# Performance work log

Measured on AMD Instinct MI355X. Metric: run time of the kernel, lower is better.

Reference implementation:

```python
import jax, jax.numpy as jnp
import numpy as np

EPS = 1e-8
BOX2D_IDX = jnp.array([0, 1, 3, 4, 6])  # x, y, dx, dy, yaw


def box2corners(box):
    # box: (..., 5) = (x, y, w, h, alpha) -> corners (..., 4, 2), CCW order
    x, y, w, h, a = (box[..., i] for i in range(5))
    tx = jnp.array([0.5, -0.5, -0.5, 0.5], box.dtype)
    ty = jnp.array([0.5, 0.5, -0.5, -0.5], box.dtype)
    x4 = tx * w[..., None]
    y4 = ty * h[..., None]
    c, s = jnp.cos(a)[..., None], jnp.sin(a)[..., None]
    rx = c * x4 - s * y4 + x[..., None]
    ry = s * x4 + c * y4 + y[..., None]
    return jnp.stack([rx, ry], axis=-1)


def edge_intersections(c1, c2):
    # all 4x4 edge-edge intersections of two quads -> pts (..., 16, 2), mask (..., 16)
    p1 = c1[..., :, None, :]
    p2 = jnp.roll(c1, -1, axis=-2)[..., :, None, :]
    q1 = c2[..., None, :, :]
    q2 = jnp.roll(c2, -1, axis=-2)[..., None, :, :]
    r = p2 - p1
    s = q2 - q1
    denom = r[..., 0] * s[..., 1] - r[..., 1] * s[..., 0]
    safe = jnp.where(jnp.abs(denom) < EPS, 1.0, denom)
    qp = q1 - p1
    t = (qp[..., 0] * s[..., 1] - qp[..., 1] * s[..., 0]) / safe
    u = (qp[..., 0] * r[..., 1] - qp[..., 1] * r[..., 0]) / safe
    mask = (jnp.abs(denom) > EPS) & (t > 0) & (t < 1) & (u > 0) & (u < 1)
    pts = jnp.where(mask[..., None], p1 + t[..., None] * r, 0.0)
    lead = pts.shape[:-3]
    return pts.reshape(lead + (16, 2)), mask.reshape(lead + (16,))


def points_in_box(pts, corners):
    # pts (..., K, 2) inside rotated quad given by corners (..., 4, 2) -> (..., K) bool
    a = corners[..., 0:1, :]
    ab = corners[..., 1:2, :] - a
    ad = corners[..., 3:4, :] - a
    ap = pts - a
    pab = jnp.sum(ap * ab, -1)
    pad = jnp.sum(ap * ad, -1)
    nab = jnp.sum(ab * ab, -1)
    nad = jnp.sum(ad * ad, -1)
    return (pab > 0) & (pab < nab) & (pad > 0) & (pad < nad)


def masked_polygon_area(verts, mask):
    # verts (..., 24, 2) candidate vertices, mask (..., 24) validity
    m = mask.astype(verts.dtype)
    num = jnp.maximum(jnp.sum(m, -1, keepdims=True), 1.0)
    mean = jnp.sum(verts * m[..., None], -2, keepdims=True) / num[..., None]
    d = verts - mean  # centered (shoelace is translation-invariant)
    ang = jnp.arctan2(d[..., 1], d[..., 0])
    # push invalid vertices to the end with stable tie-break
    ang = jnp.where(mask, ang, 1e6 + jnp.arange(24, dtype=ang.dtype))
    idx = jnp.argsort(ang, axis=-1)
    vs = jnp.take_along_axis(d, idx[..., None], axis=-2)
    ms = jnp.take_along_axis(mask, idx, axis=-1)
    v0 = vs[..., 0:1, :]
    vs = jnp.where(ms[..., None], vs, v0)  # collapse invalid onto first vertex
    nxt = jnp.roll(vs, -1, axis=-2)
    cross = vs[..., 0] * nxt[..., 1] - vs[..., 1] * nxt[..., 0]
    return 0.5 * jnp.abs(jnp.sum(cross, -1))


def rotated_iou_3d(b1, b2):
    # b1, b2: (..., 7) = (x, y, z, dx, dy, dz, yaw); elementwise-aligned IoU
    c1 = box2corners(b1[..., BOX2D_IDX])
    c2 = box2corners(b2[..., BOX2D_IDX])
    ipts, imask = edge_intersections(c1, c2)
    in1 = points_in_box(c1, c2)
    in2 = points_in_box(c2, c1)
    verts = jnp.concatenate([c1, c2, ipts], axis=-2)  # (..., 24, 2)
    mask = jnp.concatenate([in1, in2, imask], axis=-1)
    inter2d = masked_polygon_area(verts, mask)
    zmax = jnp.minimum(b1[..., 2] + 0.5 * b1[..., 5], b2[..., 2] + 0.5 * b2[..., 5])
    zmin = jnp.maximum(b1[..., 2] - 0.5 * b1[..., 5], b2[..., 2] - 0.5 * b2[..., 5])
    inter3d = inter2d * jnp.maximum(zmax - zmin, 0.0)
    v1 = b1[..., 3] * b1[..., 4] * b1[..., 5]
    v2 = b2[..., 3] * b2[..., 4] * b2[..., 5]
    return inter3d / (v1 + v2 - inter3d + EPS)


def setup_inputs() -> dict:
    key = jax.random.key(0)
    k1, k2, k3, k4, k5 = jax.random.split(key, 5)
    N = 1048576
    ctr = (jax.random.uniform(k1, (N, 3)) - 0.5) * 40.0
    dims = jax.random.uniform(k2, (N, 3)) * 2.0 + 0.5
    yaw = (jax.random.uniform(k3, (N, 1)) - 0.5) * (2.0 * np.pi)
    pred = jnp.concatenate([ctr, dims, yaw], axis=-1).astype(jnp.float32)
    noise = jax.random.normal(k4, (N, 7)) * jnp.array(
        [0.3, 0.3, 0.3, 0.2, 0.2, 0.2, 0.2], jnp.float32)
    target = pred + noise
    target = target.at[:, 3:6].set(jnp.maximum(target[:, 3:6], 0.1))
    weight = jax.random.uniform(k5, (N,), dtype=jnp.float32)
    return {"pred": pred, "target": target, "weight": weight}


def reference(pred, target, weight):
    # IoU3DLoss(with_yaw=True, reduction='mean', loss_weight=1.0)
    loss_weight = 1.0
    iou = rotated_iou_3d(pred[None, ...], target[None, ...])  # (1, N)
    iou_loss = (1.0 - iou) * weight
    return loss_weight * jnp.mean(iou_loss)
```

## Files before the change

kernel.cpp:

```cpp
#include <hip/hip_runtime.h>

#define EPS_F 1e-8f
#define EPT 4

typedef float vf4 __attribute__((ext_vector_type(4)));

__device__ __forceinline__ vf4 load4u(const float* p) {
    vf4 v;
    __builtin_memcpy(&v, p, 16);
    return v;
}

__device__ __forceinline__ float fast_rcp(float x) {
    return __builtin_amdgcn_rcpf(x);
}

__global__ void zero_out_kernel(float* out) { out[0] = 0.f; }

__device__ __forceinline__ float edge_contrib(float ax, float ay,
                                              float bx, float by,
                                              float W, float H) {
    float dx = bx - ax, dy = by - ay;
    float sdx = (fabsf(dx) < 1e-20f) ? 1e-20f : dx;
    float sdy = (fabsf(dy) < 1e-20f) ? 1e-20f : dy;
    float rdx = fast_rcp(sdx);
    float rdy = fast_rcp(sdy);

    float tA = (-W - ax) * rdx;
    float tB = ( W - ax) * rdx;
    float ta = fmaxf(fminf(tA, tB), 0.f);
    float tb = fminf(fmaxf(tA, tB), 1.f);
    tb = fmaxf(ta, tb);

    float u0 = (-H - ay) * rdy;
    float u1 = ( H - ay) * rdy;
    float tm0 = fminf(u0, u1), tm1 = fmaxf(u0, u1);
    float t1 = fminf(fmaxf(tm0, ta), tb);
    float t2 = fminf(fmaxf(tm1, ta), tb);

    float x0 = fmaf(ta, dx, ax), y0 = fmaf(ta, dy, ay);
    float x1 = fmaf(t1, dx, ax), y1 = fmaf(t1, dy, ay);
    float x2 = fmaf(t2, dx, ax), y2 = fmaf(t2, dy, ay);
    float x3 = fmaf(tb, dx, ax), y3 = fmaf(tb, dy, ay);
    float h0 = fminf(fmaxf(y0, -H), H) + H;
    float h1 = fminf(fmaxf(y1, -H), H) + H;
    float h2 = fminf(fmaxf(y2, -H), H) + H;
    float h3 = fminf(fmaxf(y3, -H), H) + H;

    return (x1 - x0) * (h0 + h1) + (x2 - x1) * (h1 + h2) + (x3 - x2) * (h2 + h3);
}

__global__ __launch_bounds__(256, 4) void iou3d_loss_kernel(
    const float* __restrict__ pred, const float* __restrict__ target,
    const float* __restrict__ weight, float* __restrict__ out,
    int N, float invN)
{
    int base = blockIdx.x * (256 * EPT) + threadIdx.x;

    vf4 A0[EPT], A1[EPT], B0[EPT], B1[EPT];
    float wgt[EPT];
    #pragma unroll
    for (int e = 0; e < EPT; ++e) {
        int i = base + e * 256;
        int j = (i < N) ? i : 0;
        long o = (long)j * 7;
        A0[e] = load4u(pred + o);
        A1[e] = load4u(pred + o + 3);
        B0[e] = load4u(target + o);
        B1[e] = load4u(target + o + 3);
        wgt[e] = (i < N) ? weight[j] : 0.f;
    }

    float val = 0.f;
    #pragma unroll
    for (int e = 0; e < EPT; ++e) {
        float s1, c1, s2, c2;
        __sincosf(A1[e].w, &s1, &c1);
        __sincosf(B1[e].w, &s2, &c2);
        float cd = c1 * c2 + s1 * s2;
        float sd = c1 * s2 - s1 * c2;
        float dxc = B0[e].x - A0[e].x, dyc = B0[e].y - A0[e].y;
        float tx =  c1 * dxc + s1 * dyc;
        float ty = -s1 * dxc + c1 * dyc;
        float W = 0.5f * A1[e].x, H = 0.5f * A1[e].y;
        float w2 = 0.5f * B1[e].x, h2 = 0.5f * B1[e].y;

        float cw = cd * w2, sw = sd * w2, ch = cd * h2, sh = sd * h2;
        float q0x =  cw - sh + tx, q0y =  sw + ch + ty;
        float q1x = -cw - sh + tx, q1y = -sw + ch + ty;
        float q2x = -cw + sh + tx, q2y = -sw - ch + ty;
        float q3x =  cw + sh + tx, q3y =  sw - ch + ty;

        float s  = edge_contrib(q0x, q0y, q1x, q1y, W, H)
                 + edge_contrib(q1x, q1y, q2x, q2y, W, H)
                 + edge_contrib(q2x, q2y, q3x, q3y, W, H)
                 + edge_contrib(q3x, q3y, q0x, q0y, W, H);
        float area = 0.5f * fabsf(s);

        float zmax = fminf(A0[e].z + 0.5f * A1[e].z, B0[e].z + 0.5f * B1[e].z);
        float zmin = fmaxf(A0[e].z - 0.5f * A1[e].z, B0[e].z - 0.5f * B1[e].z);
        float inter3d = area * fmaxf(zmax - zmin, 0.f);
        float v1 = A1[e].x * A1[e].y * A1[e].z;
        float v2 = B1[e].x * B1[e].y * B1[e].z;
        float iou = inter3d * fast_rcp(v1 + v2 - inter3d + EPS_F);
        val += (1.f - iou) * wgt[e];
    }

    #pragma unroll
    for (int off = 32; off > 0; off >>= 1) val += __shfl_down(val, off, 64);
    __shared__ float wsum[4];
    int lane = threadIdx.x & 63, wid = threadIdx.x >> 6;
    if (lane == 0) wsum[wid] = val;
    __syncthreads();
    if (threadIdx.x == 0) {
        float ssum = (wsum[0] + wsum[1] + wsum[2] + wsum[3]) * invN;
        atomicAdd(out, ssum);
    }
}

extern "C" void kernel_launch(void* const* d_in, const int* in_sizes, int n_in,
                              void* d_out, int out_size, void* d_ws, size_t ws_size,
                              hipStream_t stream) {
    const float* pred   = (const float*)d_in[0];
    const float* target = (const float*)d_in[1];
    const float* weight = (const float*)d_in[2];
    float* out = (float*)d_out;
    int N = in_sizes[2];

    zero_out_kernel<<<1, 1, 0, stream>>>(out);
    int block = 256;
    int grid = (N + block * EPT - 1) / (block * EPT);
    iou3d_loss_kernel<<<grid, block, 0, stream>>>(pred, target, weight, out,
                                                  N, 1.f / (float)N);
}
```

Baseline: 102.8 us.

## Stage pred/target slabs through LDS with coalesced 16-byte loads

```diff
diff --git a/kernel.cpp b/kernel.cpp
--- a/kernel.cpp
+++ b/kernel.cpp
@@ -1,15 +1,13 @@
 #include <hip/hip_runtime.h>
 
 #define EPS_F 1e-8f
-#define EPT 4
+#define BLOCK 256
+#define EPT 2
+#define ELEMS (BLOCK * EPT)
+#define SLAB_DW (ELEMS * 7)
+#define SLAB_CH (SLAB_DW / 4)
 
 typedef float vf4 __attribute__((ext_vector_type(4)));
-
-__device__ __forceinline__ vf4 load4u(const float* p) {
-    vf4 v;
-    __builtin_memcpy(&v, p, 16);
-    return v;
-}
 
 __device__ __forceinline__ float fast_rcp(float x) {
     return __builtin_amdgcn_rcpf(x);
@@ -50,40 +48,61 @@
     return (x1 - x0) * (h0 + h1) + (x2 - x1) * (h1 + h2) + (x3 - x2) * (h2 + h3);
 }
 
-__global__ __launch_bounds__(256, 4) void iou3d_loss_kernel(
+__global__ __launch_bounds__(BLOCK, 4) void iou3d_loss_kernel(
     const float* __restrict__ pred, const float* __restrict__ target,
     const float* __restrict__ weight, float* __restrict__ out,
     int N, float invN)
 {
-    int base = blockIdx.x * (256 * EPT) + threadIdx.x;
+    const int tid = threadIdx.x;
 
-    vf4 A0[EPT], A1[EPT], B0[EPT], B1[EPT];
+    __shared__ vf4 lds4[2 * SLAB_CH];
+    const float* ldsf = (const float*)lds4;
+
+    long blk_dw = (long)blockIdx.x * SLAB_DW;
+    long maxdw  = (long)N * 7 - 4;
+    #pragma unroll
+    for (int k = 0; k < 7; ++k) {
+        int c = k * BLOCK + tid;
+        bool isT = (c >= SLAB_CH);
+        int  cl  = isT ? c - SLAB_CH : c;
+        long gdw = blk_dw + (long)cl * 4;
+        gdw = (gdw > maxdw) ? maxdw : gdw;
+        const float* src = isT ? target : pred;
+        vf4 v;
+        __builtin_memcpy(&v, src + gdw, 16);
+        lds4[c] = v;
+    }
+
     float wgt[EPT];
+    int ibase = blockIdx.x * ELEMS + tid;
     #pragma unroll
     for (int e = 0; e < EPT; ++e) {
-        int i = base + e * 256;
-        int j = (i < N) ? i : 0;
-        long o = (long)j * 7;
-        A0[e] = load4u(pred + o);
-        A1[e] = load4u(pred + o + 3);
-        B0[e] = load4u(target + o);
-        B1[e] = load4u(target + o + 3);
+        int i = ibase + e * BLOCK;
+        int j = (i < N) ? i : N - 1;
         wgt[e] = (i < N) ? weight[j] : 0.f;
     }
+
+    __syncthreads();
 
     float val = 0.f;
     #pragma unroll
     for (int e = 0; e < EPT; ++e) {
+        int el = e * BLOCK + tid;
+        const float* p = ldsf + 7 * el;
+        const float* q = ldsf + SLAB_DW + 7 * el;
+        float a0 = p[0], a1 = p[1], a2 = p[2], a3 = p[3], a4 = p[4], a5 = p[5], a6 = p[6];
+        float b0 = q[0], b1_ = q[1], b2_ = q[2], b3 = q[3], b4 = q[4], b5 = q[5], b6 = q[6];
+
         float s1, c1, s2, c2;
-        __sincosf(A1[e].w, &s1, &c1);
-        __sincosf(B1[e].w, &s2, &c2);
+        __sincosf(a6, &s1, &c1);
+        __sincosf(b6, &s2, &c2);
         float cd = c1 * c2 + s1 * s2;
         float sd = c1 * s2 - s1 * c2;
-        float dxc = B0[e].x - A0[e].x, dyc = B0[e].y - A0[e].y;
+        float dxc = b0 - a0, dyc = b1_ - a1;
         float tx =  c1 * dxc + s1 * dyc;
         float ty = -s1 * dxc + c1 * dyc;
-        float W = 0.5f * A1[e].x, H = 0.5f * A1[e].y;
-        float w2 = 0.5f * B1[e].x, h2 = 0.5f * B1[e].y;
+        float W = 0.5f * a3, H = 0.5f * a4;
+        float w2 = 0.5f * b3, h2 = 0.5f * b4;
 
         float cw = cd * w2, sw = sd * w2, ch = cd * h2, sh = sd * h2;
         float q0x =  cw - sh + tx, q0y =  sw + ch + ty;
@@ -97,11 +116,11 @@
                  + edge_contrib(q3x, q3y, q0x, q0y, W, H);
         float area = 0.5f * fabsf(s);
 
-        float zmax = fminf(A0[e].z + 0.5f * A1[e].z, B0[e].z + 0.5f * B1[e].z);
-        float zmin = fmaxf(A0[e].z - 0.5f * A1[e].z, B0[e].z - 0.5f * B1[e].z);
+        float zmax = fminf(a2 + 0.5f * a5, b2_ + 0.5f * b5);
+        float zmin = fmaxf(a2 - 0.5f * a5, b2_ - 0.5f * b5);
         float inter3d = area * fmaxf(zmax - zmin, 0.f);
-        float v1 = A1[e].x * A1[e].y * A1[e].z;
-        float v2 = B1[e].x * B1[e].y * B1[e].z;
+        float v1 = a3 * a4 * a5;
+        float v2 = b3 * b4 * b5;
         float iou = inter3d * fast_rcp(v1 + v2 - inter3d + EPS_F);
         val += (1.f - iou) * wgt[e];
     }
@@ -109,10 +128,10 @@
     #pragma unroll
     for (int off = 32; off > 0; off >>= 1) val += __shfl_down(val, off, 64);
     __shared__ float wsum[4];
-    int lane = threadIdx.x & 63, wid = threadIdx.x >> 6;
+    int lane = tid & 63, wid = tid >> 6;
     if (lane == 0) wsum[wid] = val;
     __syncthreads();
-    if (threadIdx.x == 0) {
+    if (tid == 0) {
         float ssum = (wsum[0] + wsum[1] + wsum[2] + wsum[3]) * invN;
         atomicAdd(out, ssum);
     }
@@ -128,8 +147,7 @@
     int N = in_sizes[2];
 
     zero_out_kernel<<<1, 1, 0, stream>>>(out);
-    int block = 256;
-    int grid = (N + block * EPT - 1) / (block * EPT);
-    iou3d_loss_kernel<<<grid, block, 0, stream>>>(pred, target, weight, out,
+    int grid = (N + ELEMS - 1) / ELEMS;
+    iou3d_loss_kernel<<<grid, BLOCK, 0, stream>>>(pred, target, weight, out,
                                                   N, 1.f / (float)N);
 }
```

New measurement: 112.3 us. 1.09x slower.
